# Kernel optimization log

Measured on AMD Instinct MI355X. Metric: run time of the kernel, lower is better.

The kernel has to match this reference:

```python
import jax, jax.numpy as jnp
import numpy as np
import itertools

EPS = 1e-6
OUT = 1024            # out_size[0]
RRNG = (16.0, 16.0)   # local sampling region per column (rrange)


def setup_inputs() -> dict:
    key = jax.random.key(0)
    ks = jax.random.split(key, 6)
    b, n, c, g, rad, rank = 8, 4096, 32, 4, 4, 2
    k = n // c
    in_size = 1024
    rng = jnp.array([float(OUT), float(in_size)])
    # continuous index tuples, strictly inside [0, dim-1)
    means = jax.random.uniform(ks[0], (b, n, rank)) * (rng - 1.0)
    sigmas = jax.random.uniform(ks[1], (b, n, rank)) * 0.5 + 0.1
    values = jax.random.normal(ks[2], (b, n))
    x = jax.random.normal(ks[3], (b, in_size))
    sampled_u = jax.random.uniform(ks[4], (b, k, c, g, rank))
    rr_u = jax.random.uniform(ks[5], (b, k, c, rad, rank))
    return {"x": x, "means": means, "sigmas": sigmas, "values": values,
            "sampled_u": sampled_u, "rr_u": rr_u}


def _generate_integer_tuples(means, sampled_u, rr_u, rng, rrng):
    # means: (b,k,c,rank)
    b, k, c, rank = means.shape
    # floor/ceil combinatorics: itertools.product([True, False], repeat=rank)
    fm = jnp.asarray([[int(v) for v in bits]
                      for bits in itertools.product([True, False], repeat=rank)],
                     dtype=bool)                       # (2^rank, rank)
    m = means[:, :, :, None, :]                         # (b,k,c,1,rank)
    neighbor = jnp.where(fm[None, None, None], jnp.floor(m), jnp.ceil(m))
    neighbor = jnp.broadcast_to(neighbor, (b, k, c, 2 ** rank, rank)).astype(jnp.int32)
    # global uniform samples over the full index range
    sampled = jnp.floor(sampled_u * (1.0 - EPS) * rng).astype(jnp.int32)
    # local uniform samples in a window of size rrng around round(means)
    mns = jnp.round(means)[:, :, :, None, :]
    lower = mns - rrng * 0.5
    upper = mns + rrng * 0.5
    lower = jnp.where(lower < 0.0, 0.0, lower)
    lower = jnp.where(upper > rng, rng - rrng, lower)
    rr = jnp.floor(rr_u * (1.0 - EPS) * rrng + lower).astype(jnp.int32)
    allints = jnp.concatenate([neighbor, sampled, rr], axis=3)  # (b,k,c,L,rank)
    return allints.reshape(b, k, -1, rank)                      # l = c*L


def _densities(points, means, sigmas):
    # points: (b,k,l,rank)  means/sigmas: (b,k,c,rank) -> (b,k,l,c)
    inv = jnp.sqrt(1.0 / (EPS + sigmas))
    diff = (points[:, :, :, None, :] - means[:, :, None, :, :]) * inv[:, :, None, :, :]
    return jnp.exp(-0.5 * jnp.sum(diff * diff, axis=-1))


def _mark_dups(ids):
    # ids: (b,k,l) scalar-encoded tuples; True = later occurrence of a duplicate
    # within the same (b,k) chunk context. Stable sort keeps first occurrence.
    order = jnp.argsort(ids, axis=-1)
    s = jnp.take_along_axis(ids, order, axis=-1)
    dup_s = jnp.concatenate([jnp.zeros(s.shape[:-1] + (1,), dtype=bool),
                             s[..., 1:] == s[..., :-1]], axis=-1)
    inv = jnp.argsort(order, axis=-1)
    return jnp.take_along_axis(dup_s, inv, axis=-1)


def reference(x, means, sigmas, values, sampled_u, rr_u):
    b, n, rank = means.shape
    _, k, c, g, _ = sampled_u.shape
    in_size = x.shape[1]
    rng = jnp.array([OUT, in_size], dtype=x.dtype)
    rrng = jnp.array(RRNG, dtype=x.dtype)

    means = means.reshape(b, k, c, rank)
    sigmas = sigmas.reshape(b, k, c, rank)
    values = values.reshape(b, k, c)

    ints = _generate_integer_tuples(means, sampled_u, rr_u, rng, rrng)  # (b,k,l,rank)
    indfl = ints.astype(x.dtype)

    dups = _mark_dups(ints[..., 0] * in_size + ints[..., 1])            # (b,k,l)
    props = _densities(indfl, means, sigmas)                            # (b,k,l,c)
    props = jnp.where(dups[..., None], 0.0, props)
    props = props / jnp.sum(props, axis=2, keepdims=True)

    vals = jnp.sum(props * values[:, :, None, :], axis=3)               # (b,k,l)

    idx = ints.reshape(b, -1, rank)
    v = vals.reshape(b, -1)
    bidx = jnp.arange(b)[:, None]
    # sparse contraction: out[b, i0] += v * x[b, i1]
    contrib = v * x[bidx, idx[..., 1]]
    out = jnp.zeros((b, OUT), x.dtype).at[bidx, idx[..., 0]].add(contrib)
    return out
```

## Files before the change

kernel.cpp:

```cpp
#include <hip/hip_runtime.h>

#define CQ 32
#define KQ 128
#define NPTS 384
#define OUTN 1024
#define BQ 8
#define NACC (BQ * OUTN)
#define HSZ 1024
#define WS_NEED ((size_t)BQ * KQ * OUTN * sizeof(float))

__global__ void zero_out(float* __restrict__ out) {
    int i = blockIdx.x * blockDim.x + threadIdx.x;
    if (i < NACC) out[i] = 0.0f;
}

__device__ __forceinline__ float wave_red_dpp(float v) {
#define DPPADD(ctrl)                                                              \
    {                                                                             \
        int t_ = __builtin_amdgcn_update_dpp(0, __float_as_int(v), (ctrl), 0xF,   \
                                             0xF, true);                          \
        v += __int_as_float(t_);                                                  \
    }
    DPPADD(0x111)
    DPPADD(0x112)
    DPPADD(0x114)
    DPPADD(0x118)
    DPPADD(0x142)
    DPPADD(0x143)
#undef DPPADD
    return v;
}

__global__ __launch_bounds__(NPTS) void sparse_part(
    const float* __restrict__ x,
    const float* __restrict__ means,
    const float* __restrict__ sigmas,
    const float* __restrict__ values,
    const float* __restrict__ su,
    const float* __restrict__ ru,
    float* __restrict__ dst,
    int use_ws)
{
    const int k = blockIdx.x, b = blockIdx.y;
    const int tid = threadIdx.x;
    const int lane = tid & 63, wid = tid >> 6;
    const int gk = b * KQ + k;
    const int c = tid / 12, j = tid % 12;
    const int cb = gk * CQ + c;
    const float CEPS = (float)(1.0 - 1e-6);

    __shared__ float4 gp[CQ];
    __shared__ float valc[CQ];
    __shared__ int htab[HSZ];
    __shared__ float part[6][CQ];
    __shared__ float wnorm[CQ];
    __shared__ float acc[OUTN];

    const float2 mcb = *(const float2*)&means[cb * 2];
    float2 uu = make_float2(0.0f, 0.0f);
    if (j >= 8)       uu = *(const float2*)&ru[(cb * 4 + (j - 8)) * 2];
    else if (j >= 4)  uu = *(const float2*)&su[(cb * 4 + (j - 4)) * 2];
    float2 mg, sg; float vv = 0.0f;
    if (tid < CQ) {
        int cbs = gk * CQ + tid;
        mg = *(const float2*)&means[cbs * 2];
        sg = *(const float2*)&sigmas[cbs * 2];
        vv = values[cbs];
    }

    for (int i = tid; i < HSZ; i += NPTS) htab[i] = -1;
    if (use_ws) {
        for (int i = tid; i < OUTN; i += NPTS) acc[i] = 0.0f;
    }
    if (tid < CQ) {
        float i0 = __fsqrt_rn(__fdiv_rn(1.0f, __fadd_rn(1e-6f, sg.x)));
        float i1 = __fsqrt_rn(__fdiv_rn(1.0f, __fadd_rn(1e-6f, sg.y)));
        gp[tid] = make_float4(mg.x, mg.y, i0, i1);
        valc[tid] = vv;
    }

    const float mm0 = mcb.x, mm1 = mcb.y;
    int p0, p1;
    if (j < 4) {
        p0 = (int)((j >= 2) ? ceilf(mm0) : floorf(mm0));
        p1 = (int)((j & 1) ? ceilf(mm1) : floorf(mm1));
    } else if (j < 8) {
        p0 = (int)floorf(__fmul_rn(__fmul_rn(uu.x, CEPS), 1024.0f));
        p1 = (int)floorf(__fmul_rn(__fmul_rn(uu.y, CEPS), 1024.0f));
    } else {
        float mn0 = rintf(mm0), mn1 = rintf(mm1);
        float lo0 = mn0 - 8.0f; if (lo0 < 0.0f) lo0 = 0.0f; if (mn0 + 8.0f > 1024.0f) lo0 = 1008.0f;
        float lo1 = mn1 - 8.0f; if (lo1 < 0.0f) lo1 = 0.0f; if (mn1 + 8.0f > 1024.0f) lo1 = 1008.0f;
        p0 = (int)floorf(__fadd_rn(__fmul_rn(__fmul_rn(uu.x, CEPS), 16.0f), lo0));
        p1 = (int)floorf(__fadd_rn(__fmul_rn(__fmul_rn(uu.y, CEPS), 16.0f), lo1));
    }
    __syncthreads();

    const int myid = p0 * 1024 + p1;
    int slot = (int)(((unsigned)myid * 2654435761u) >> 22);
    bool dup = false;
    while (true) {
        int prev = atomicCAS(&htab[slot], -1, myid);
        if (prev == -1) break;
        if (prev == myid) { dup = true; break; }
        slot = (slot + 1) & (HSZ - 1);
    }

    const float pf0 = (float)p0, pf1 = (float)p1;
    float pr[CQ];
    #pragma unroll
    for (int cc = 0; cc < CQ; ++cc) {
        float4 g = gp[cc];
        float d0 = (pf0 - g.x) * g.z;
        float d1 = (pf1 - g.y) * g.w;
        float e = __expf(-0.5f * (d0 * d0 + d1 * d1));
        pr[cc] = dup ? 0.0f : e;
    }

    #pragma unroll
    for (int cc = 0; cc < CQ; ++cc) {
        float v = wave_red_dpp(pr[cc]);
        if (lane == 63) part[wid][cc] = v;
    }
    __syncthreads();
    if (tid < CQ) {
        float s = 0.0f;
        #pragma unroll
        for (int w = 0; w < 6; ++w) s += part[w][tid];
        wnorm[tid] = valc[tid] / s;
    }
    __syncthreads();

    if (!dup) {
        float vals = 0.0f;
        #pragma unroll
        for (int cc = 0; cc < CQ; ++cc) vals += pr[cc] * wnorm[cc];
        int g1 = p1 < 0 ? 0 : (p1 > OUTN - 1 ? OUTN - 1 : p1);
        float contrib = vals * x[b * OUTN + g1];
        if (p0 >= 0 && p0 < OUTN) {
            if (use_ws) atomicAdd(&acc[p0], contrib);
            else        atomicAdd(&dst[b * OUTN + p0], contrib);
        }
    }

    if (use_ws) {
        __syncthreads();
        float* w = dst + (size_t)gk * OUTN;
        for (int i = tid; i < OUTN; i += NPTS) w[i] = acc[i];
    }
}

__global__ void reduce_ws(const float* __restrict__ ws, float* __restrict__ out) {
    int t = blockIdx.x * blockDim.x + threadIdx.x;
    if (t >= NACC) return;
    int b = t >> 10, cidx = t & (OUTN - 1);
    const float* p = ws + (size_t)b * KQ * OUTN + cidx;
    float s0 = 0.0f, s1 = 0.0f, s2 = 0.0f, s3 = 0.0f;
    #pragma unroll
    for (int k = 0; k < KQ; k += 4) {
        s0 += p[(size_t)(k + 0) * OUTN];
        s1 += p[(size_t)(k + 1) * OUTN];
        s2 += p[(size_t)(k + 2) * OUTN];
        s3 += p[(size_t)(k + 3) * OUTN];
    }
    out[t] = (s0 + s1) + (s2 + s3);
}

extern "C" void kernel_launch(void* const* d_in, const int* in_sizes, int n_in,
                              void* d_out, int out_size, void* d_ws, size_t ws_size,
                              hipStream_t stream) {
    const float* x      = (const float*)d_in[0];
    const float* means  = (const float*)d_in[1];
    const float* sigmas = (const float*)d_in[2];
    const float* values = (const float*)d_in[3];
    const float* su     = (const float*)d_in[4];
    const float* ru     = (const float*)d_in[5];
    float* out = (float*)d_out;
    float* ws  = (float*)d_ws;

    if (ws_size >= WS_NEED) {
        sparse_part<<<dim3(KQ, BQ), dim3(NPTS), 0, stream>>>(
            x, means, sigmas, values, su, ru, ws, 1);
        reduce_ws<<<dim3((NACC + 127) / 128), dim3(128), 0, stream>>>(ws, out);
    } else {
        zero_out<<<dim3((NACC + 255) / 256), dim3(256), 0, stream>>>(out);
        sparse_part<<<dim3(KQ, BQ), dim3(NPTS), 0, stream>>>(
            x, means, sigmas, values, su, ru, out, 0);
    }
}
```

Baseline: 96.51 us.

## Map each (b,k) group to a single wave with six points per lane

Each (batch, k) group, which used to be a 384-thread block, is now handled by one 64-lane wave that owns six points per lane, and four independent groups share a block. Per-column normalisation uses a DPP wave reduction plus a shuffle instead of cross-wave shared-memory partials and two block barriers. Gaussian parameters are broadcast with shuffles rather than staged in shared memory. This removes __syncthreads and shared-memory traffic, but puts six times the serial work on each lane and uses more registers and shared memory per block.

```diff
diff --git a/kernel.cpp b/kernel.cpp
--- a/kernel.cpp
+++ b/kernel.cpp
@@ -2,12 +2,15 @@
 
 #define CQ 32
 #define KQ 128
-#define NPTS 384
 #define OUTN 1024
 #define BQ 8
 #define NACC (BQ * OUTN)
 #define HSZ 1024
-#define WS_NEED ((size_t)BQ * KQ * OUTN * sizeof(float))
+#define PPL 6
+#define WPB 4
+#define NGROUP (BQ * KQ)
+#define NBLK (NGROUP / WPB)
+#define WS_NEED ((size_t)NGROUP * OUTN * sizeof(float))
 
 __global__ void zero_out(float* __restrict__ out) {
     int i = blockIdx.x * blockDim.x + threadIdx.x;
@@ -31,7 +34,7 @@
     return v;
 }
 
-__global__ __launch_bounds__(NPTS) void sparse_part(
+__global__ __launch_bounds__(WPB * 64) void sparse_wave(
     const float* __restrict__ x,
     const float* __restrict__ means,
     const float* __restrict__ sigmas,
@@ -41,112 +44,123 @@
     float* __restrict__ dst,
     int use_ws)
 {
-    const int k = blockIdx.x, b = blockIdx.y;
-    const int tid = threadIdx.x;
-    const int lane = tid & 63, wid = tid >> 6;
-    const int gk = b * KQ + k;
-    const int c = tid / 12, j = tid % 12;
-    const int cb = gk * CQ + c;
+    const int lane = threadIdx.x & 63;
+    const int w = threadIdx.x >> 6;
+    const int gk = blockIdx.x * WPB + w;
+    const int b = gk >> 7;
     const float CEPS = (float)(1.0 - 1e-6);
 
-    __shared__ float4 gp[CQ];
-    __shared__ float valc[CQ];
-    __shared__ int htab[HSZ];
-    __shared__ float part[6][CQ];
-    __shared__ float wnorm[CQ];
-    __shared__ float acc[OUTN];
-
-    const float2 mcb = *(const float2*)&means[cb * 2];
-    float2 uu = make_float2(0.0f, 0.0f);
-    if (j >= 8)       uu = *(const float2*)&ru[(cb * 4 + (j - 8)) * 2];
-    else if (j >= 4)  uu = *(const float2*)&su[(cb * 4 + (j - 4)) * 2];
-    float2 mg, sg; float vv = 0.0f;
-    if (tid < CQ) {
-        int cbs = gk * CQ + tid;
-        mg = *(const float2*)&means[cbs * 2];
-        sg = *(const float2*)&sigmas[cbs * 2];
-        vv = values[cbs];
-    }
-
-    for (int i = tid; i < HSZ; i += NPTS) htab[i] = -1;
+    __shared__ int htab[WPB][HSZ];
+    __shared__ float acc[WPB][OUTN];
+
+    #pragma unroll
+    for (int i = 0; i < HSZ / 64; ++i) htab[w][i * 64 + lane] = -1;
     if (use_ws) {
-        for (int i = tid; i < OUTN; i += NPTS) acc[i] = 0.0f;
-    }
-    if (tid < CQ) {
-        float i0 = __fsqrt_rn(__fdiv_rn(1.0f, __fadd_rn(1e-6f, sg.x)));
-        float i1 = __fsqrt_rn(__fdiv_rn(1.0f, __fadd_rn(1e-6f, sg.y)));
-        gp[tid] = make_float4(mg.x, mg.y, i0, i1);
-        valc[tid] = vv;
-    }
-
-    const float mm0 = mcb.x, mm1 = mcb.y;
-    int p0, p1;
-    if (j < 4) {
-        p0 = (int)((j >= 2) ? ceilf(mm0) : floorf(mm0));
-        p1 = (int)((j & 1) ? ceilf(mm1) : floorf(mm1));
-    } else if (j < 8) {
-        p0 = (int)floorf(__fmul_rn(__fmul_rn(uu.x, CEPS), 1024.0f));
-        p1 = (int)floorf(__fmul_rn(__fmul_rn(uu.y, CEPS), 1024.0f));
-    } else {
-        float mn0 = rintf(mm0), mn1 = rintf(mm1);
-        float lo0 = mn0 - 8.0f; if (lo0 < 0.0f) lo0 = 0.0f; if (mn0 + 8.0f > 1024.0f) lo0 = 1008.0f;
-        float lo1 = mn1 - 8.0f; if (lo1 < 0.0f) lo1 = 0.0f; if (mn1 + 8.0f > 1024.0f) lo1 = 1008.0f;
-        p0 = (int)floorf(__fadd_rn(__fmul_rn(__fmul_rn(uu.x, CEPS), 16.0f), lo0));
-        p1 = (int)floorf(__fadd_rn(__fmul_rn(__fmul_rn(uu.y, CEPS), 16.0f), lo1));
-    }
-    __syncthreads();
-
-    const int myid = p0 * 1024 + p1;
-    int slot = (int)(((unsigned)myid * 2654435761u) >> 22);
-    bool dup = false;
-    while (true) {
-        int prev = atomicCAS(&htab[slot], -1, myid);
-        if (prev == -1) break;
-        if (prev == myid) { dup = true; break; }
-        slot = (slot + 1) & (HSZ - 1);
-    }
-
-    const float pf0 = (float)p0, pf1 = (float)p1;
-    float pr[CQ];
+        #pragma unroll
+        for (int i = 0; i < OUTN / 64; ++i) acc[w][i * 64 + lane] = 0.0f;
+    }
+
+    float pm0 = 0.f, pm1 = 0.f, pi0 = 0.f, pi1 = 0.f, pv = 0.f;
+    if (lane < CQ) {
+        int cb = gk * CQ + lane;
+        float2 mg = *(const float2*)&means[cb * 2];
+        float2 sg = *(const float2*)&sigmas[cb * 2];
+        pm0 = mg.x; pm1 = mg.y;
+        pi0 = __fsqrt_rn(__fdiv_rn(1.0f, __fadd_rn(1e-6f, sg.x)));
+        pi1 = __fsqrt_rn(__fdiv_rn(1.0f, __fadd_rn(1e-6f, sg.y)));
+        pv  = values[cb];
+    }
+
+    int p0[PPL], p1[PPL];
+    #pragma unroll
+    for (int i = 0; i < PPL; ++i) {
+        const int pt = i * 64 + lane;
+        const int c = pt / 12, j = pt % 12;
+        const float mm0 = __shfl(pm0, c), mm1 = __shfl(pm1, c);
+        int q0, q1;
+        if (j < 4) {
+            q0 = (int)((j >= 2) ? ceilf(mm0) : floorf(mm0));
+            q1 = (int)((j & 1) ? ceilf(mm1) : floorf(mm1));
+        } else if (j < 8) {
+            float2 uu = *(const float2*)&su[(gk * CQ + c) * 8 + (j - 4) * 2];
+            q0 = (int)floorf(__fmul_rn(__fmul_rn(uu.x, CEPS), 1024.0f));
+            q1 = (int)floorf(__fmul_rn(__fmul_rn(uu.y, CEPS), 1024.0f));
+        } else {
+            float2 uu = *(const float2*)&ru[(gk * CQ + c) * 8 + (j - 8) * 2];
+            float mn0 = rintf(mm0), mn1 = rintf(mm1);
+            float lo0 = mn0 - 8.0f; if (lo0 < 0.0f) lo0 = 0.0f; if (mn0 + 8.0f > 1024.0f) lo0 = 1008.0f;
+            float lo1 = mn1 - 8.0f; if (lo1 < 0.0f) lo1 = 0.0f; if (mn1 + 8.0f > 1024.0f) lo1 = 1008.0f;
+            q0 = (int)floorf(__fadd_rn(__fmul_rn(__fmul_rn(uu.x, CEPS), 16.0f), lo0));
+            q1 = (int)floorf(__fadd_rn(__fmul_rn(__fmul_rn(uu.y, CEPS), 16.0f), lo1));
+        }
+        p0[i] = q0; p1[i] = q1;
+    }
+
+    float xv[PPL];
+    #pragma unroll
+    for (int i = 0; i < PPL; ++i) {
+        int g1 = p1[i] < 0 ? 0 : (p1[i] > OUTN - 1 ? OUTN - 1 : p1[i]);
+        xv[i] = x[b * OUTN + g1];
+    }
+
+    unsigned dupm = 0u;
+    #pragma unroll
+    for (int i = 0; i < PPL; ++i) {
+        const int myid = p0[i] * 1024 + p1[i];
+        int slot = (int)(((unsigned)myid * 2654435761u) >> 22);
+        while (true) {
+            int prev = atomicCAS(&htab[w][slot], -1, myid);
+            if (prev == -1) break;
+            if (prev == myid) { dupm |= (1u << i); break; }
+            slot = (slot + 1) & (HSZ - 1);
+        }
+    }
+
+    const float pf0[PPL] = {(float)p0[0], (float)p0[1], (float)p0[2],
+                            (float)p0[3], (float)p0[4], (float)p0[5]};
+    const float pf1[PPL] = {(float)p1[0], (float)p1[1], (float)p1[2],
+                            (float)p1[3], (float)p1[4], (float)p1[5]};
+
+    float vals[PPL] = {0.f, 0.f, 0.f, 0.f, 0.f, 0.f};
     #pragma unroll
     for (int cc = 0; cc < CQ; ++cc) {
-        float4 g = gp[cc];
-        float d0 = (pf0 - g.x) * g.z;
-        float d1 = (pf1 - g.y) * g.w;
-        float e = __expf(-0.5f * (d0 * d0 + d1 * d1));
-        pr[cc] = dup ? 0.0f : e;
-    }
-
-    #pragma unroll
-    for (int cc = 0; cc < CQ; ++cc) {
-        float v = wave_red_dpp(pr[cc]);
-        if (lane == 63) part[wid][cc] = v;
-    }
-    __syncthreads();
-    if (tid < CQ) {
-        float s = 0.0f;
-        #pragma unroll
-        for (int w = 0; w < 6; ++w) s += part[w][tid];
-        wnorm[tid] = valc[tid] / s;
-    }
-    __syncthreads();
-
-    if (!dup) {
-        float vals = 0.0f;
-        #pragma unroll
-        for (int cc = 0; cc < CQ; ++cc) vals += pr[cc] * wnorm[cc];
-        int g1 = p1 < 0 ? 0 : (p1 > OUTN - 1 ? OUTN - 1 : p1);
-        float contrib = vals * x[b * OUTN + g1];
-        if (p0 >= 0 && p0 < OUTN) {
-            if (use_ws) atomicAdd(&acc[p0], contrib);
-            else        atomicAdd(&dst[b * OUTN + p0], contrib);
+        const float m0 = __shfl(pm0, cc), m1 = __shfl(pm1, cc);
+        const float i0 = __shfl(pi0, cc), i1 = __shfl(pi1, cc);
+        const float vv = __shfl(pv, cc);
+        float e[PPL];
+        float s = 0.f;
+        #pragma unroll
+        for (int i = 0; i < PPL; ++i) {
+            float d0 = (pf0[i] - m0) * i0;
+            float d1 = (pf1[i] - m1) * i1;
+            float t = __expf(-0.5f * (d0 * d0 + d1 * d1));
+            t = ((dupm >> i) & 1u) ? 0.0f : t;
+            e[i] = t; s += t;
+        }
+        s = wave_red_dpp(s);
+        const float ss = __shfl(s, 63);
+        const float wn = vv / ss;
+        #pragma unroll
+        for (int i = 0; i < PPL; ++i) vals[i] += e[i] * wn;
+    }
+
+    #pragma unroll
+    for (int i = 0; i < PPL; ++i) {
+        if (!((dupm >> i) & 1u) && p0[i] >= 0 && p0[i] < OUTN) {
+            float contrib = vals[i] * xv[i];
+            if (use_ws) atomicAdd(&acc[w][p0[i]], contrib);
+            else        atomicAdd(&dst[b * OUTN + p0[i]], contrib);
         }
     }
 
     if (use_ws) {
-        __syncthreads();
-        float* w = dst + (size_t)gk * OUTN;
-        for (int i = tid; i < OUTN; i += NPTS) w[i] = acc[i];
+        float* wsp = dst + (size_t)gk * OUTN;
+        #pragma unroll
+        for (int ii = 0; ii < OUTN / 256; ++ii) {
+            int idx = ii * 256 + lane * 4;
+            float4 v = *(const float4*)&acc[w][idx];
+            *(float4*)&wsp[idx] = v;
+        }
     }
 }
 
@@ -179,12 +193,12 @@
     float* ws  = (float*)d_ws;
 
     if (ws_size >= WS_NEED) {
-        sparse_part<<<dim3(KQ, BQ), dim3(NPTS), 0, stream>>>(
+        sparse_wave<<<dim3(NBLK), dim3(WPB * 64), 0, stream>>>(
             x, means, sigmas, values, su, ru, ws, 1);
         reduce_ws<<<dim3((NACC + 127) / 128), dim3(128), 0, stream>>>(ws, out);
     } else {
         zero_out<<<dim3((NACC + 255) / 256), dim3(256), 0, stream>>>(out);
-        sparse_part<<<dim3(KQ, BQ), dim3(NPTS), 0, stream>>>(
+        sparse_wave<<<dim3(NBLK), dim3(WPB * 64), 0, stream>>>(
             x, means, sigmas, values, su, ru, out, 0);
     }
 }
```

Measured after the change: 90.49 us. 1.07x faster.
